# Kernel tuning notes

Measured on AMD Instinct MI355X. Metric: run time of the kernel, lower is better.

Reference implementation:

```python
import jax, jax.numpy as jnp
import numpy as np

D_MODEL = 1024
NUM_HEADS = 16
D_K = D_MODEL // NUM_HEADS


def setup_inputs() -> dict:
    key = jax.random.key(0)
    ks = jax.random.split(key, 9)
    B, S = 4, 2048
    s = 1.0 / np.sqrt(D_MODEL)
    return {
        "x": jax.random.normal(ks[0], (B, S, D_MODEL), dtype=jnp.float32),
        "Wq": jax.random.uniform(ks[1], (D_MODEL, D_MODEL), jnp.float32, -s, s),
        "bq": jax.random.uniform(ks[2], (D_MODEL,), jnp.float32, -s, s),
        "Wk": jax.random.uniform(ks[3], (D_MODEL, D_MODEL), jnp.float32, -s, s),
        "bk": jax.random.uniform(ks[4], (D_MODEL,), jnp.float32, -s, s),
        "Wv": jax.random.uniform(ks[5], (D_MODEL, D_MODEL), jnp.float32, -s, s),
        "bv": jax.random.uniform(ks[6], (D_MODEL,), jnp.float32, -s, s),
        "Wo": jax.random.uniform(ks[7], (D_MODEL, D_MODEL), jnp.float32, -s, s),
        "bo": jax.random.uniform(ks[8], (D_MODEL,), jnp.float32, -s, s),
    }


def reference(x, Wq, bq, Wk, bk, Wv, bv, Wo, bo):
    B, S, D = x.shape
    H, dk = NUM_HEADS, D_K

    def proj(W, b):
        # [B,S,D] -> [B,H,S,dk]  (torch Linear: x @ W^T + b)
        y = jnp.einsum('bsd,ed->bse', x, W) + b
        return y.reshape(B, S, H, dk).transpose(0, 2, 1, 3)

    Q = proj(Wq, bq)
    K = proj(Wk, bk)
    V = proj(Wv, bv)

    scale = 1.0 / jnp.sqrt(jnp.asarray(dk, x.dtype))
    scores = jnp.einsum('bhqd,bhkd->bhqk', Q, K) * scale  # [B,H,S,S]
    attn = jax.nn.softmax(scores, axis=-1)
    # dropout is identity in eval mode
    out = jnp.einsum('bhqk,bhkd->bhqd', attn, V)  # [B,H,S,dk]
    out = out.transpose(0, 2, 1, 3).reshape(B, S, D)
    return jnp.einsum('bsd,ed->bse', out, Wo) + bo
```

## Files before the change

### kernel.cpp

```cpp
#include <hip/hip_runtime.h>


typedef unsigned short u16;
typedef unsigned int u32;
typedef __attribute__((ext_vector_type(8))) short bf16x8;
typedef __attribute__((ext_vector_type(4))) float f32x4;
typedef __attribute__((ext_vector_type(4))) unsigned short u16x4;
typedef __attribute__((ext_vector_type(8))) unsigned short u16x8;

#define SEQ    2048
#define DMODEL 1024
#define NHEAD  16
#define DK     64
#define BATCH  4
#define MROWS  (BATCH * SEQ)
#define LCF    0.18033688011112042f

__device__ __forceinline__ u16 f2bf(float f) {
  unsigned int u = __float_as_uint(f);
  u += 0x7fffu + ((u >> 16) & 1u);
  return (u16)(u >> 16);
}

__device__ __forceinline__ void gload_lds16(const void* g, void* l) {
  __builtin_amdgcn_global_load_lds((const __attribute__((address_space(1))) void*)g,
                                   (__attribute__((address_space(3))) void*)l,
                                   16, 0, 0);
}

__global__ __launch_bounds__(256) void cvt_all(const float* __restrict__ x,
                                               const float* __restrict__ w0,
                                               const float* __restrict__ w1,
                                               const float* __restrict__ w2,
                                               const float* __restrict__ w3,
                                               u16* xb, u16* o0, u16* o1, u16* o2, u16* o3) {
  const int NX4 = MROWS * DMODEL / 4;
  int i = blockIdx.x * 256 + threadIdx.x;
  const float* src; u16* dst; int off;
  if (i < NX4) { src = x; dst = xb; off = i; }
  else {
    int j = i - NX4;
    int wi = j >> 18; off = j & 0x3FFFF;
    src = wi == 0 ? w0 : wi == 1 ? w1 : wi == 2 ? w2 : w3;
    dst = wi == 0 ? o0 : wi == 1 ? o1 : wi == 2 ? o2 : o3;
  }
  float4 v = ((const float4*)src)[off];
  u16x4 o;
  o.x = f2bf(v.x); o.y = f2bf(v.y); o.z = f2bf(v.z); o.w = f2bf(v.w);
  ((u16x4*)dst)[off] = o;
}

template <int OUT_F32>
__device__ __forceinline__ void gemm_body(const u16* __restrict__ A,
                                          const u16* __restrict__ Bw,
                                          const float* __restrict__ bias,
                                          void* __restrict__ outp,
                                          int bm, int bn, int M, int N, int K,
                                          float scale, int vt_mode,
                                          u16* As, u16* Bs) {
  const int t = threadIdx.x, w = t >> 6, l = t & 63;
  const int wr = (w >> 1) * 64, wc = (w & 1) * 64;
  const int lrow = l & 15, kgrp = l >> 4;
  const int r_in = l >> 3;
  const int c_in = ((l & 7) ^ r_in) * 8;
  const int sw = lrow & 7;

  f32x4 acc[4][4] = {};

  for (int kt = 0; kt < K; kt += 64) {
#pragma unroll
    for (int it = 0; it < 4; ++it) {
      const int chunk = w * 4 + it;
      const int row = chunk * 8 + r_in;
      gload_lds16(A  + (size_t)(bm * 128 + row) * K + kt + c_in, (char*)As + chunk * 1024);
      gload_lds16(Bw + (size_t)(bn * 128 + row) * K + kt + c_in, (char*)Bs + chunk * 1024);
    }
    __syncthreads();
#pragma unroll
    for (int kc = 0; kc < 2; ++kc) {
      bf16x8 af[4], bfr[4];
      const int slot = (kc * 4 + kgrp) ^ sw;
#pragma unroll
      for (int m = 0; m < 4; ++m)
        af[m] = *(const bf16x8*)&As[(wr + m * 16 + lrow) * 64 + slot * 8];
#pragma unroll
      for (int n = 0; n < 4; ++n)
        bfr[n] = *(const bf16x8*)&Bs[(wc + n * 16 + lrow) * 64 + slot * 8];
#pragma unroll
      for (int m = 0; m < 4; ++m)
#pragma unroll
        for (int n = 0; n < 4; ++n)
          acc[m][n] = __builtin_amdgcn_mfma_f32_16x16x32_bf16(af[m], bfr[n], acc[m][n], 0, 0, 0);
    }
    __syncthreads();
  }

  const int cr0 = bm * 128 + wr, cc0 = bn * 128 + wc;
  if (!OUT_F32 && vt_mode) {
    const int s0 = (bm & 15) * 128 + wr + kgrp * 4;
    u16* vtp = (u16*)outp + (size_t)(bm >> 4) * 1024 * 2048;
#pragma unroll
    for (int n = 0; n < 4; ++n) {
      const int col = cc0 + n * 16 + lrow;
      const float bv = bias[col];
#pragma unroll
      for (int m = 0; m < 4; ++m) {
        u16x4 pk;
#pragma unroll
        for (int r = 0; r < 4; ++r) pk[r] = f2bf(acc[m][n][r] + bv);
        *(u16x4*)&vtp[(size_t)col * 2048 + s0 + m * 16] = pk;
      }
    }
    return;
  }
#pragma unroll
  for (int n = 0; n < 4; ++n) {
    const int col = cc0 + n * 16 + lrow;
    const float bv = bias[col];
#pragma unroll
    for (int m = 0; m < 4; ++m) {
#pragma unroll
      for (int r = 0; r < 4; ++r) {
        const int row = cr0 + m * 16 + kgrp * 4 + r;
        const float v = (acc[m][n][r] + bv) * scale;
        if (OUT_F32) ((float*)outp)[(size_t)row * N + col] = v;
        else         ((u16*)outp)[(size_t)row * N + col] = f2bf(v);
      }
    }
  }
}

__global__ __launch_bounds__(256) void gemm_bt_f32(const u16* __restrict__ A,
                                                   const u16* __restrict__ Bw,
                                                   const float* __restrict__ bias,
                                                   float* __restrict__ outp) {
  __shared__ u16 As[128 * 64];
  __shared__ u16 Bs[128 * 64];
  const int wg = blockIdx.x;
  const int xcd = wg & 7, local = wg >> 3;
  const int lm = local & 7, bn = local >> 3;
  const int bm = xcd * 8 + lm;
  gemm_body<1>(A, Bw, bias, outp, bm, bn, MROWS, DMODEL, DMODEL, 1.0f, 0, As, Bs);
}

__global__ __launch_bounds__(256) void gemm_qkv(const u16* __restrict__ A,
                                                const u16* __restrict__ W0,
                                                const u16* __restrict__ W1,
                                                const u16* __restrict__ W2,
                                                const float* __restrict__ b0,
                                                const float* __restrict__ b1,
                                                const float* __restrict__ b2,
                                                u16* o0, u16* o1, u16* vt) {
  __shared__ u16 As[128 * 64];
  __shared__ u16 Bs[128 * 64];
  const int wg = blockIdx.x;
  const int xcd = wg & 7, local = wg >> 3;
  const int lm = local & 7, lnsel = local >> 3;
  const int bm = xcd * 8 + lm;
  const int sel = lnsel >> 3, bn = lnsel & 7;
  const u16* Bw = sel == 0 ? W0 : sel == 1 ? W1 : W2;
  const float* bias = sel == 0 ? b0 : sel == 1 ? b1 : b2;
  u16* outp = sel == 0 ? o0 : sel == 1 ? o1 : vt;
  const float scale = sel == 0 ? LCF : 1.0f;
  gemm_body<0>(A, Bw, bias, outp, bm, bn, MROWS, DMODEL, DMODEL, scale,
               sel == 2 ? 1 : 0, As, Bs);
}

__global__ __launch_bounds__(256, 4) void attn_kernel(const u16* __restrict__ Qg,
                                                      const u16* __restrict__ Kg,
                                                      const u16* __restrict__ Vt,
                                                      u16* __restrict__ Og) {
  __shared__ u16 Ks[2][64 * 64];
  __shared__ u16 Vs[2][64 * 64];

  const int t = threadIdx.x, w = t >> 6, l = t & 63;
  const int lrow = l & 15, kgrp = l >> 4;
  const int sw = lrow & 7;

  const int id = blockIdx.x;
  const int swzid = (id & 7) * 128 + (id >> 3);
  const int qt = swzid & 15, bh = swzid >> 4;
  const int b = bh >> 4, h = bh & 15;
  const size_t base  = (size_t)b * SEQ * DMODEL + h * DK;
  const size_t vbase = (size_t)bh * DK * SEQ;
  const int r_in = l >> 3;
  const int c_in = ((l & 7) ^ r_in) * 8;

  int kro[2];
#pragma unroll
  for (int it = 0; it < 2; ++it) {
    const int p = (w * 2 + it) * 8 + r_in;
    const int n_ = p >> 4, g_ = (p >> 2) & 3, rr = p & 3;
    kro[it] = (n_ >> 1) * 32 + g_ * 8 + (n_ & 1) * 4 + rr;
  }

  const int qr = qt * 128 + w * 32;
  bf16x8 aq[2][2];
#pragma unroll
  for (int rg = 0; rg < 2; ++rg) {
    const u16* qp = Qg + base + (size_t)(qr + rg * 16 + lrow) * DMODEL + kgrp * 8;
    aq[rg][0] = *(const bf16x8*)qp;
    aq[rg][1] = *(const bf16x8*)(qp + 32);
  }

  f32x4 o_acc[2][4] = {};
  float lsum[2] = {};

#define STAGE(kt_, buf_)                                                        \
  {                                                                             \
    const int k0_ = (kt_) * 64;                                                 \
    _Pragma("unroll")                                                           \
    for (int it = 0; it < 2; ++it) {                                            \
      const int chunk = w * 2 + it;                                             \
      const int r = chunk * 8 + r_in;                                           \
      gload_lds16(Kg + base + (size_t)(k0_ + kro[it]) * DMODEL + c_in,          \
                  (char*)&Ks[buf_][0] + chunk * 1024);                          \
      gload_lds16(Vt + vbase + (size_t)r * SEQ + k0_ + c_in,                    \
                  (char*)&Vs[buf_][0] + chunk * 1024);                          \
    }                                                                           \
  }

  STAGE(0, 0);

  for (int kt = 0; kt < SEQ / 64; ++kt) {
    const int buf = kt & 1;
    __syncthreads();
    if (kt + 1 < SEQ / 64) STAGE(kt + 1, buf ^ 1);

    f32x4 sc[2][4] = {};
    __builtin_amdgcn_s_setprio(1);
#pragma unroll
    for (int kc = 0; kc < 2; ++kc) {
      const int slot = (kc * 4 + kgrp) ^ sw;
#pragma unroll
      for (int n = 0; n < 4; ++n) {
        bf16x8 bk = *(const bf16x8*)&Ks[buf][(n * 16 + lrow) * 64 + slot * 8];
        sc[0][n] = __builtin_amdgcn_mfma_f32_16x16x32_bf16(bk, aq[0][kc], sc[0][n], 0, 0, 0);
        sc[1][n] = __builtin_amdgcn_mfma_f32_16x16x32_bf16(bk, aq[1][kc], sc[1][n], 0, 0, 0);
      }
    }
    __builtin_amdgcn_s_setprio(0);

    bf16x8 pa[2][2];
#pragma unroll
    for (int rg = 0; rg < 2; ++rg) {
      u32 pk[4][2];
      float lp = 0.0f;
#pragma unroll
      for (int n = 0; n < 4; ++n) {
        const float p0 = __builtin_amdgcn_exp2f(sc[rg][n][0]);
        const float p1 = __builtin_amdgcn_exp2f(sc[rg][n][1]);
        const float p2 = __builtin_amdgcn_exp2f(sc[rg][n][2]);
        const float p3 = __builtin_amdgcn_exp2f(sc[rg][n][3]);
        lp += (p0 + p1) + (p2 + p3);
        asm("v_cvt_pk_bf16_f32 %0, %1, %2" : "=v"(pk[n][0]) : "v"(p0), "v"(p1));
        asm("v_cvt_pk_bf16_f32 %0, %1, %2" : "=v"(pk[n][1]) : "v"(p2), "v"(p3));
      }
      lsum[rg] += lp;
      union { u32 u[4]; bf16x8 v; } f0, f1;
      f0.u[0] = pk[0][0]; f0.u[1] = pk[0][1]; f0.u[2] = pk[1][0]; f0.u[3] = pk[1][1];
      f1.u[0] = pk[2][0]; f1.u[1] = pk[2][1]; f1.u[2] = pk[3][0]; f1.u[3] = pk[3][1];
      pa[rg][0] = f0.v;
      pa[rg][1] = f1.v;
    }

    __builtin_amdgcn_s_setprio(1);
#pragma unroll
    for (int kc = 0; kc < 2; ++kc) {
      const int slot = (kc * 4 + kgrp) ^ sw;
#pragma unroll
      for (int n = 0; n < 4; ++n) {
        bf16x8 bv = *(const bf16x8*)&Vs[buf][(n * 16 + lrow) * 64 + slot * 8];
        o_acc[0][n] = __builtin_amdgcn_mfma_f32_16x16x32_bf16(pa[0][kc], bv, o_acc[0][n], 0, 0, 0);
        o_acc[1][n] = __builtin_amdgcn_mfma_f32_16x16x32_bf16(pa[1][kc], bv, o_acc[1][n], 0, 0, 0);
      }
    }
    __builtin_amdgcn_s_setprio(0);
  }
#undef STAGE

#pragma unroll
  for (int rg = 0; rg < 2; ++rg) {
    float Lq = lsum[rg];
    Lq += __shfl_xor(Lq, 16);
    Lq += __shfl_xor(Lq, 32);
#pragma unroll
    for (int r = 0; r < 4; ++r) {
      const float inv = 1.0f / __shfl(Lq, kgrp * 4 + r);
      const int row = qr + rg * 16 + kgrp * 4 + r;
#pragma unroll
      for (int n = 0; n < 4; ++n)
        Og[base + (size_t)row * DMODEL + n * 16 + lrow] = f2bf(o_acc[rg][n][r] * inv);
    }
  }
}

extern "C" void kernel_launch(void* const* d_in, const int* in_sizes, int n_in,
                              void* d_out, int out_size, void* d_ws, size_t ws_size,
                              hipStream_t stream) {
  const float* x  = (const float*)d_in[0];
  const float* Wq = (const float*)d_in[1];
  const float* bq = (const float*)d_in[2];
  const float* Wk = (const float*)d_in[3];
  const float* bk = (const float*)d_in[4];
  const float* Wv = (const float*)d_in[5];
  const float* bv = (const float*)d_in[6];
  const float* Wo = (const float*)d_in[7];
  const float* bo = (const float*)d_in[8];
  float* out = (float*)d_out;

  const size_t XB   = (size_t)MROWS * DMODEL * 2;
  const size_t WB   = (size_t)DMODEL * DMODEL * 2;
  const size_t NEED = XB * 5 + WB * 4;
  if (ws_size < NEED) return;

  char* ws = (char*)d_ws;
  u16* xb  = (u16*)(ws);
  u16* wqb = (u16*)(ws + XB);
  u16* wkb = (u16*)(ws + XB + WB);
  u16* wvb = (u16*)(ws + XB + 2 * WB);
  u16* wob = (u16*)(ws + XB + 3 * WB);
  u16* qb  = (u16*)(ws + XB + 4 * WB);
  u16* kb  = (u16*)(ws + 2 * XB + 4 * WB);
  u16* vt  = (u16*)(ws + 3 * XB + 4 * WB);
  u16* ab  = (u16*)(ws + 4 * XB + 4 * WB);

  const int NCVT = (MROWS * DMODEL / 4) + DMODEL * DMODEL;
  cvt_all<<<NCVT / 256, 256, 0, stream>>>(x, Wq, Wk, Wv, Wo, xb, wqb, wkb, wvb, wob);

  gemm_qkv<<<dim3(1536), 256, 0, stream>>>(xb, wqb, wkb, wvb,
                                           bq, bk, bv, qb, kb, vt);

  attn_kernel<<<dim3(1024), 256, 0, stream>>>(qb, kb, vt, ab);

  gemm_bt_f32<<<dim3(512), 256, 0, stream>>>(ab, wob, bo, out);
}
```

Measured before the change: 175.2 us.

## Switch attention to 32x32 MFMA and software-pipeline QK, softmax and PV across tiles

Replaces the 16x16x32 MFMA tiling in the attention kernel with 32x32x16 MFMAs, which changes the K-row permutation and how Q fragments and outputs are laid out. The main loop is restructured so the QK product of tile k+1 is issued alongside the PV product of tile k, with softmax for one tile overlapping matrix work on another. V gets a triple buffer to support the deeper pipeline. The aim is better MFMA utilisation and hiding exp latency, at the cost of extra LDS and higher register pressure.

```diff
diff --git a/kernel.cpp b/kernel.cpp
--- a/kernel.cpp
+++ b/kernel.cpp
@@ -5,6 +5,7 @@
 typedef unsigned int u32;
 typedef __attribute__((ext_vector_type(8))) short bf16x8;
 typedef __attribute__((ext_vector_type(4))) float f32x4;
+typedef __attribute__((ext_vector_type(16))) float f32x16;
 typedef __attribute__((ext_vector_type(4))) unsigned short u16x4;
 typedef __attribute__((ext_vector_type(8))) unsigned short u16x8;
 
@@ -171,17 +172,16 @@
                                                       const u16* __restrict__ Vt,
                                                       u16* __restrict__ Og) {
   __shared__ u16 Ks[2][64 * 64];
-  __shared__ u16 Vs[2][64 * 64];
+  __shared__ u16 Vs[3][64 * 64];
 
   const int t = threadIdx.x, w = t >> 6, l = t & 63;
-  const int lrow = l & 15, kgrp = l >> 4;
-  const int sw = lrow & 7;
+  const int l31 = l & 31, h = l >> 5, l7 = l & 7;
 
   const int id = blockIdx.x;
   const int swzid = (id & 7) * 128 + (id >> 3);
   const int qt = swzid & 15, bh = swzid >> 4;
-  const int b = bh >> 4, h = bh & 15;
-  const size_t base  = (size_t)b * SEQ * DMODEL + h * DK;
+  const int b = bh >> 4, hd = bh & 15;
+  const size_t base  = (size_t)b * SEQ * DMODEL + hd * DK;
   const size_t vbase = (size_t)bh * DK * SEQ;
   const int r_in = l >> 3;
   const int c_in = ((l & 7) ^ r_in) * 8;
@@ -190,23 +190,22 @@
 #pragma unroll
   for (int it = 0; it < 2; ++it) {
     const int p = (w * 2 + it) * 8 + r_in;
-    const int n_ = p >> 4, g_ = (p >> 2) & 3, rr = p & 3;
-    kro[it] = (n_ >> 1) * 32 + g_ * 8 + (n_ & 1) * 4 + rr;
+    const int n_ = p >> 5, b_ = (p >> 3) & 3, h_ = (p >> 2) & 1, c_ = p & 3;
+    kro[it] = 16 * (2 * n_ + (b_ & 1)) + 8 * h_ + 4 * (b_ >> 1) + c_;
   }
 
   const int qr = qt * 128 + w * 32;
-  bf16x8 aq[2][2];
-#pragma unroll
-  for (int rg = 0; rg < 2; ++rg) {
-    const u16* qp = Qg + base + (size_t)(qr + rg * 16 + lrow) * DMODEL + kgrp * 8;
-    aq[rg][0] = *(const bf16x8*)qp;
-    aq[rg][1] = *(const bf16x8*)(qp + 32);
-  }
-
-  f32x4 o_acc[2][4] = {};
-  float lsum[2] = {};
-
-#define STAGE(kt_, buf_)                                                        \
+  bf16x8 aq[4];
+#pragma unroll
+  for (int kd = 0; kd < 4; ++kd)
+    aq[kd] = *(const bf16x8*)(Qg + base + (size_t)(qr + l31) * DMODEL + kd * 16 + h * 8);
+
+  f32x16 o_acc[2] = {};
+  f32x16 sc[2];
+  bf16x8 paA[4], paB[4];
+  float lsum = 0.0f;
+
+#define STAGE(kt_, kb_, vb_)                                                    \
   {                                                                             \
     const int k0_ = (kt_) * 64;                                                 \
     _Pragma("unroll")                                                           \
@@ -214,83 +213,124 @@
       const int chunk = w * 2 + it;                                             \
       const int r = chunk * 8 + r_in;                                           \
       gload_lds16(Kg + base + (size_t)(k0_ + kro[it]) * DMODEL + c_in,          \
-                  (char*)&Ks[buf_][0] + chunk * 1024);                          \
+                  (char*)&Ks[kb_][0] + chunk * 1024);                           \
       gload_lds16(Vt + vbase + (size_t)r * SEQ + k0_ + c_in,                    \
-                  (char*)&Vs[buf_][0] + chunk * 1024);                          \
-    }                                                                           \
-  }
-
-  STAGE(0, 0);
-
-  for (int kt = 0; kt < SEQ / 64; ++kt) {
-    const int buf = kt & 1;
+                  (char*)&Vs[vb_][0] + chunk * 1024);                           \
+    }                                                                           \
+  }
+
+#define QK_BLOCK(KB)                                                            \
+  {                                                                             \
+    f32x16 z = {};                                                              \
+    sc[0] = z; sc[1] = z;                                                       \
+    __builtin_amdgcn_s_setprio(1);                                              \
+    _Pragma("unroll")                                                           \
+    for (int kd = 0; kd < 4; ++kd) {                                            \
+      const int slot = ((2 * kd + h) ^ l7) * 8;                                 \
+      bf16x8 k0f = *(const bf16x8*)&Ks[KB][l31 * 64 + slot];                    \
+      bf16x8 k1f = *(const bf16x8*)&Ks[KB][(32 + l31) * 64 + slot];             \
+      sc[0] = __builtin_amdgcn_mfma_f32_32x32x16_bf16(k0f, aq[kd], sc[0], 0, 0, 0); \
+      sc[1] = __builtin_amdgcn_mfma_f32_32x32x16_bf16(k1f, aq[kd], sc[1], 0, 0, 0); \
+    }                                                                           \
+    __builtin_amdgcn_s_setprio(0);                                              \
+  }
+
+#define SM_BLOCK(PA)                                                            \
+  {                                                                             \
+    float P0[16], P1[16];                                                       \
+    float lp = 0.0f;                                                            \
+    _Pragma("unroll")                                                           \
+    for (int e = 0; e < 16; ++e) {                                              \
+      P0[e] = __builtin_amdgcn_exp2f(sc[0][e]);                                 \
+      P1[e] = __builtin_amdgcn_exp2f(sc[1][e]);                                 \
+      lp += P0[e] + P1[e];                                                      \
+    }                                                                           \
+    lsum += lp;                                                                 \
+    _Pragma("unroll")                                                           \
+    for (int ks = 0; ks < 4; ++ks) {                                            \
+      const int g0 = (ks & 1) * 4, g2 = 8 + (ks & 1) * 4;                       \
+      union { u32 u[4]; bf16x8 v; } tmp;                                        \
+      if (ks < 2) {                                                             \
+        asm("v_cvt_pk_bf16_f32 %0, %1, %2" : "=v"(tmp.u[0]) : "v"(P0[g0+0]), "v"(P0[g0+1])); \
+        asm("v_cvt_pk_bf16_f32 %0, %1, %2" : "=v"(tmp.u[1]) : "v"(P0[g0+2]), "v"(P0[g0+3])); \
+        asm("v_cvt_pk_bf16_f32 %0, %1, %2" : "=v"(tmp.u[2]) : "v"(P0[g2+0]), "v"(P0[g2+1])); \
+        asm("v_cvt_pk_bf16_f32 %0, %1, %2" : "=v"(tmp.u[3]) : "v"(P0[g2+2]), "v"(P0[g2+3])); \
+      } else {                                                                  \
+        asm("v_cvt_pk_bf16_f32 %0, %1, %2" : "=v"(tmp.u[0]) : "v"(P1[g0+0]), "v"(P1[g0+1])); \
+        asm("v_cvt_pk_bf16_f32 %0, %1, %2" : "=v"(tmp.u[1]) : "v"(P1[g0+2]), "v"(P1[g0+3])); \
+        asm("v_cvt_pk_bf16_f32 %0, %1, %2" : "=v"(tmp.u[2]) : "v"(P1[g2+0]), "v"(P1[g2+1])); \
+        asm("v_cvt_pk_bf16_f32 %0, %1, %2" : "=v"(tmp.u[3]) : "v"(P1[g2+2]), "v"(P1[g2+3])); \
+      }                                                                         \
+      PA[ks] = tmp.v;                                                           \
+    }                                                                           \
+  }
+
+#define PV_BLOCK(PA, VB)                                                        \
+  {                                                                             \
+    __builtin_amdgcn_s_setprio(1);                                              \
+    _Pragma("unroll")                                                           \
+    for (int ks = 0; ks < 4; ++ks) {                                            \
+      const int slot = ((2 * ks + h) ^ l7) * 8;                                 \
+      bf16x8 v0 = *(const bf16x8*)&Vs[VB][l31 * 64 + slot];                     \
+      bf16x8 v1 = *(const bf16x8*)&Vs[VB][(32 + l31) * 64 + slot];              \
+      o_acc[0] = __builtin_amdgcn_mfma_f32_32x32x16_bf16(PA[ks], v0, o_acc[0], 0, 0, 0); \
+      o_acc[1] = __builtin_amdgcn_mfma_f32_32x32x16_bf16(PA[ks], v1, o_acc[1], 0, 0, 0); \
+    }                                                                           \
+    __builtin_amdgcn_s_setprio(0);                                              \
+  }
+
+  STAGE(0, 0, 0);
+  __syncthreads();
+  STAGE(1, 1, 1);
+  QK_BLOCK(0);
+  SM_BLOCK(paA);
+
+  int vi_w = 2, vi_r = 0;
+#pragma unroll 1
+  for (int jj = 0; jj < 15; ++jj) {
+    const int tA = 1 + 2 * jj;
     __syncthreads();
-    if (kt + 1 < SEQ / 64) STAGE(kt + 1, buf ^ 1);
-
-    f32x4 sc[2][4] = {};
-    __builtin_amdgcn_s_setprio(1);
-#pragma unroll
-    for (int kc = 0; kc < 2; ++kc) {
-      const int slot = (kc * 4 + kgrp) ^ sw;
-#pragma unroll
-      for (int n = 0; n < 4; ++n) {
-        bf16x8 bk = *(const bf16x8*)&Ks[buf][(n * 16 + lrow) * 64 + slot * 8];
-        sc[0][n] = __builtin_amdgcn_mfma_f32_16x16x32_bf16(bk, aq[0][kc], sc[0][n], 0, 0, 0);
-        sc[1][n] = __builtin_amdgcn_mfma_f32_16x16x32_bf16(bk, aq[1][kc], sc[1][n], 0, 0, 0);
-      }
-    }
-    __builtin_amdgcn_s_setprio(0);
-
-    bf16x8 pa[2][2];
-#pragma unroll
-    for (int rg = 0; rg < 2; ++rg) {
-      u32 pk[4][2];
-      float lp = 0.0f;
-#pragma unroll
-      for (int n = 0; n < 4; ++n) {
-        const float p0 = __builtin_amdgcn_exp2f(sc[rg][n][0]);
-        const float p1 = __builtin_amdgcn_exp2f(sc[rg][n][1]);
-        const float p2 = __builtin_amdgcn_exp2f(sc[rg][n][2]);
-        const float p3 = __builtin_amdgcn_exp2f(sc[rg][n][3]);
-        lp += (p0 + p1) + (p2 + p3);
-        asm("v_cvt_pk_bf16_f32 %0, %1, %2" : "=v"(pk[n][0]) : "v"(p0), "v"(p1));
-        asm("v_cvt_pk_bf16_f32 %0, %1, %2" : "=v"(pk[n][1]) : "v"(p2), "v"(p3));
-      }
-      lsum[rg] += lp;
-      union { u32 u[4]; bf16x8 v; } f0, f1;
-      f0.u[0] = pk[0][0]; f0.u[1] = pk[0][1]; f0.u[2] = pk[1][0]; f0.u[3] = pk[1][1];
-      f1.u[0] = pk[2][0]; f1.u[1] = pk[2][1]; f1.u[2] = pk[3][0]; f1.u[3] = pk[3][1];
-      pa[rg][0] = f0.v;
-      pa[rg][1] = f1.v;
-    }
-
-    __builtin_amdgcn_s_setprio(1);
-#pragma unroll
-    for (int kc = 0; kc < 2; ++kc) {
-      const int slot = (kc * 4 + kgrp) ^ sw;
-#pragma unroll
-      for (int n = 0; n < 4; ++n) {
-        bf16x8 bv = *(const bf16x8*)&Vs[buf][(n * 16 + lrow) * 64 + slot * 8];
-        o_acc[0][n] = __builtin_amdgcn_mfma_f32_16x16x32_bf16(pa[0][kc], bv, o_acc[0][n], 0, 0, 0);
-        o_acc[1][n] = __builtin_amdgcn_mfma_f32_16x16x32_bf16(pa[1][kc], bv, o_acc[1][n], 0, 0, 0);
-      }
-    }
-    __builtin_amdgcn_s_setprio(0);
-  }
+    STAGE(tA + 1, 0, vi_w);
+    vi_w = (vi_w == 2) ? 0 : vi_w + 1;
+    QK_BLOCK(1);
+    PV_BLOCK(paA, vi_r);
+    vi_r = (vi_r == 2) ? 0 : vi_r + 1;
+    SM_BLOCK(paB);
+
+    __syncthreads();
+    STAGE(tA + 2, 1, vi_w);
+    vi_w = (vi_w == 2) ? 0 : vi_w + 1;
+    QK_BLOCK(0);
+    PV_BLOCK(paB, vi_r);
+    vi_r = (vi_r == 2) ? 0 : vi_r + 1;
+    SM_BLOCK(paA);
+  }
+  __syncthreads();
+  QK_BLOCK(1);
+  PV_BLOCK(paA, vi_r);
+  vi_r = (vi_r == 2) ? 0 : vi_r + 1;
+  SM_BLOCK(paB);
+  PV_BLOCK(paB, vi_r);
+
 #undef STAGE
-
-#pragma unroll
-  for (int rg = 0; rg < 2; ++rg) {
-    float Lq = lsum[rg];
-    Lq += __shfl_xor(Lq, 16);
-    Lq += __shfl_xor(Lq, 32);
-#pragma unroll
-    for (int r = 0; r < 4; ++r) {
-      const float inv = 1.0f / __shfl(Lq, kgrp * 4 + r);
-      const int row = qr + rg * 16 + kgrp * 4 + r;
-#pragma unroll
-      for (int n = 0; n < 4; ++n)
-        Og[base + (size_t)row * DMODEL + n * 16 + lrow] = f2bf(o_acc[rg][n][r] * inv);
+#undef QK_BLOCK
+#undef SM_BLOCK
+#undef PV_BLOCK
+
+  float Lq = lsum + __shfl_xor(lsum, 32);
+  const float inv = 1.0f / Lq;
+  float invq[16];
+#pragma unroll
+  for (int r = 0; r < 16; ++r) {
+    const int q = (r & 3) + 8 * (r >> 2) + 4 * h;
+    invq[r] = __shfl(inv, q);
+  }
+#pragma unroll
+  for (int n = 0; n < 2; ++n) {
+#pragma unroll
+    for (int r = 0; r < 16; ++r) {
+      const int q = (r & 3) + 8 * (r >> 2) + 4 * h;
+      Og[base + (size_t)(qr + q) * DMODEL + 32 * n + l31] = f2bf(o_acc[n][r] * invq[r]);
     }
   }
 }
```

Result: slower. 263.0 us (+50.1%).

## Double attention query tile per block to reuse K/V tiles across more rows

Applied to the files above, without the earlier changes.

Each attention block now processes 256 query rows (64 per wave) instead of 128, halving the grid to 512 blocks, and K/V fragments are loaded from LDS once per tile and reused across four row groups. This halves global K/V traffic and the LDS reads per MFMA. In exchange it raises register pressure (occupancy hint lowered to 2) and leaves fewer blocks to fill the CUs.

```diff
diff --git a/kernel.cpp b/kernel.cpp
--- a/kernel.cpp
+++ b/kernel.cpp
@@ -166,7 +166,7 @@
                sel == 2 ? 1 : 0, As, Bs);
 }
 
-__global__ __launch_bounds__(256, 4) void attn_kernel(const u16* __restrict__ Qg,
+__global__ __launch_bounds__(256, 2) void attn_kernel(const u16* __restrict__ Qg,
                                                       const u16* __restrict__ Kg,
                                                       const u16* __restrict__ Vt,
                                                       u16* __restrict__ Og) {
@@ -178,8 +178,8 @@
   const int sw = lrow & 7;
 
   const int id = blockIdx.x;
-  const int swzid = (id & 7) * 128 + (id >> 3);
-  const int qt = swzid & 15, bh = swzid >> 4;
+  const int swzid = (id & 7) * 64 + (id >> 3);
+  const int qt = swzid & 7, bh = swzid >> 3;
   const int b = bh >> 4, h = bh & 15;
   const size_t base  = (size_t)b * SEQ * DMODEL + h * DK;
   const size_t vbase = (size_t)bh * DK * SEQ;
@@ -194,17 +194,19 @@
     kro[it] = (n_ >> 1) * 32 + g_ * 8 + (n_ & 1) * 4 + rr;
   }
 
-  const int qr = qt * 128 + w * 32;
-  bf16x8 aq[2][2];
-#pragma unroll
-  for (int rg = 0; rg < 2; ++rg) {
+  const int qr = qt * 256 + w * 64;
+  bf16x8 aq[4][2];
+#pragma unroll
+  for (int rg = 0; rg < 4; ++rg) {
     const u16* qp = Qg + base + (size_t)(qr + rg * 16 + lrow) * DMODEL + kgrp * 8;
     aq[rg][0] = *(const bf16x8*)qp;
     aq[rg][1] = *(const bf16x8*)(qp + 32);
   }
 
-  f32x4 o_acc[2][4] = {};
-  float lsum[2] = {};
+  f32x4 o_acc[4][4] = {};
+  float lsum[4] = {};
+  const int slot0 = (kgrp ^ sw) * 8;
+  const int slot1 = ((4 + kgrp) ^ sw) * 8;
 
 #define STAGE(kt_, buf_)                                                        \
   {                                                                             \
@@ -227,31 +229,34 @@
     __syncthreads();
     if (kt + 1 < SEQ / 64) STAGE(kt + 1, buf ^ 1);
 
-    f32x4 sc[2][4] = {};
-    __builtin_amdgcn_s_setprio(1);
-#pragma unroll
-    for (int kc = 0; kc < 2; ++kc) {
-      const int slot = (kc * 4 + kgrp) ^ sw;
-#pragma unroll
-      for (int n = 0; n < 4; ++n) {
-        bf16x8 bk = *(const bf16x8*)&Ks[buf][(n * 16 + lrow) * 64 + slot * 8];
-        sc[0][n] = __builtin_amdgcn_mfma_f32_16x16x32_bf16(bk, aq[0][kc], sc[0][n], 0, 0, 0);
-        sc[1][n] = __builtin_amdgcn_mfma_f32_16x16x32_bf16(bk, aq[1][kc], sc[1][n], 0, 0, 0);
-      }
-    }
-    __builtin_amdgcn_s_setprio(0);
-
-    bf16x8 pa[2][2];
-#pragma unroll
-    for (int rg = 0; rg < 2; ++rg) {
+    bf16x8 kf0[4], kf1[4];
+#pragma unroll
+    for (int n = 0; n < 4; ++n) {
+      kf0[n] = *(const bf16x8*)&Ks[buf][(n * 16 + lrow) * 64 + slot0];
+      kf1[n] = *(const bf16x8*)&Ks[buf][(n * 16 + lrow) * 64 + slot1];
+    }
+
+    bf16x8 pa[4][2];
+#pragma unroll
+    for (int rg = 0; rg < 4; ++rg) {
+      f32x4 sc[4] = {};
+      __builtin_amdgcn_s_setprio(1);
+#pragma unroll
+      for (int n = 0; n < 4; ++n)
+        sc[n] = __builtin_amdgcn_mfma_f32_16x16x32_bf16(kf0[n], aq[rg][0], sc[n], 0, 0, 0);
+#pragma unroll
+      for (int n = 0; n < 4; ++n)
+        sc[n] = __builtin_amdgcn_mfma_f32_16x16x32_bf16(kf1[n], aq[rg][1], sc[n], 0, 0, 0);
+      __builtin_amdgcn_s_setprio(0);
+
       u32 pk[4][2];
       float lp = 0.0f;
 #pragma unroll
       for (int n = 0; n < 4; ++n) {
-        const float p0 = __builtin_amdgcn_exp2f(sc[rg][n][0]);
-        const float p1 = __builtin_amdgcn_exp2f(sc[rg][n][1]);
-        const float p2 = __builtin_amdgcn_exp2f(sc[rg][n][2]);
-        const float p3 = __builtin_amdgcn_exp2f(sc[rg][n][3]);
+        const float p0 = __builtin_amdgcn_exp2f(sc[n][0]);
+        const float p1 = __builtin_amdgcn_exp2f(sc[n][1]);
+        const float p2 = __builtin_amdgcn_exp2f(sc[n][2]);
+        const float p3 = __builtin_amdgcn_exp2f(sc[n][3]);
         lp += (p0 + p1) + (p2 + p3);
         asm("v_cvt_pk_bf16_f32 %0, %1, %2" : "=v"(pk[n][0]) : "v"(p0), "v"(p1));
         asm("v_cvt_pk_bf16_f32 %0, %1, %2" : "=v"(pk[n][1]) : "v"(p2), "v"(p3));
@@ -264,23 +269,29 @@
       pa[rg][1] = f1.v;
     }
 
+    bf16x8 vf0[4], vf1[4];
+#pragma unroll
+    for (int n = 0; n < 4; ++n) {
+      vf0[n] = *(const bf16x8*)&Vs[buf][(n * 16 + lrow) * 64 + slot0];
+      vf1[n] = *(const bf16x8*)&Vs[buf][(n * 16 + lrow) * 64 + slot1];
+    }
+
     __builtin_amdgcn_s_setprio(1);
 #pragma unroll
-    for (int kc = 0; kc < 2; ++kc) {
-      const int slot = (kc * 4 + kgrp) ^ sw;
-#pragma unroll
-      for (int n = 0; n < 4; ++n) {
-        bf16x8 bv = *(const bf16x8*)&Vs[buf][(n * 16 + lrow) * 64 + slot * 8];
-        o_acc[0][n] = __builtin_amdgcn_mfma_f32_16x16x32_bf16(pa[0][kc], bv, o_acc[0][n], 0, 0, 0);
-        o_acc[1][n] = __builtin_amdgcn_mfma_f32_16x16x32_bf16(pa[1][kc], bv, o_acc[1][n], 0, 0, 0);
-      }
+    for (int rg = 0; rg < 4; ++rg) {
+#pragma unroll
+      for (int n = 0; n < 4; ++n)
+        o_acc[rg][n] = __builtin_amdgcn_mfma_f32_16x16x32_bf16(pa[rg][0], vf0[n], o_acc[rg][n], 0, 0, 0);
+#pragma unroll
+      for (int n = 0; n < 4; ++n)
+        o_acc[rg][n] = __builtin_amdgcn_mfma_f32_16x16x32_bf16(pa[rg][1], vf1[n], o_acc[rg][n], 0, 0, 0);
     }
     __builtin_amdgcn_s_setprio(0);
   }
 #undef STAGE
 
 #pragma unroll
-  for (int rg = 0; rg < 2; ++rg) {
+  for (int rg = 0; rg < 4; ++rg) {
     float Lq = lsum[rg];
     Lq += __shfl_xor(Lq, 16);
     Lq += __shfl_xor(Lq, 32);
@@ -331,7 +342,7 @@
   gemm_qkv<<<dim3(1536), 256, 0, stream>>>(xb, wqb, wkb, wvb,
                                            bq, bk, bv, qb, kb, vt);
 
-  attn_kernel<<<dim3(1024), 256, 0, stream>>>(qb, kb, vt, ab);
+  attn_kernel<<<dim3(512), 256, 0, stream>>>(qb, kb, vt, ab);
 
   gemm_bt_f32<<<dim3(512), 256, 0, stream>>>(ab, wob, bo, out);
 }
```

Measured after the change: 173.6 us, median of 2. Within noise of the previous version (-0.9%).
